# Kernel optimization log

Measured on AMD Instinct MI355X. Metric: run time of the kernel, lower is better.

The kernel has to match this reference:

```python
import jax, jax.numpy as jnp
import numpy as np

N, IN, HID, OUT, HD = 512, 256, 256, 256, 64  # n_agents, in_dim, hid_dim, out_dim, head_dim (out_dim // n_heads)


def _mlp2(x, w1, b1, w2, b2):
    return jax.nn.relu(x @ w1.T + b1) @ w2.T + b2


def setup_inputs():
    key = jax.random.key(0)
    ks = jax.random.split(key, 32)
    p = lambda i, shape: jax.random.normal(ks[i], shape, dtype=jnp.float32) * 0.05
    V = jax.random.normal(ks[0], (N, IN), dtype=jnp.float32)
    adj = jax.random.randint(ks[1], (N, N), 0, 2, dtype=jnp.int32)
    adj = adj.at[jnp.arange(N), jnp.arange(N)].set(1)  # self-loops so no softmax row is all -inf
    prev_hidden = jax.random.normal(ks[2], (N, HID), dtype=jnp.float32)
    return {
        "V": V, "adj": adj, "prev_hidden": prev_hidden,
        "W1": p(3, (HID, IN)), "sa0": p(4, (HID,)), "sa1": p(5, (HID,)),
        "ce_w1": p(6, (HID, 2 * IN)), "ce_b1": p(7, (HID,)), "ce_w2": p(8, (HD, HID)), "ce_b2": p(9, (HD,)),
        "ca0": p(10, (HD,)), "ca1": p(11, (HD,)),
        "te_w1": p(12, (HID, IN + HID)), "te_b1": p(13, (HID,)), "te_w2": p(14, (HD, HID)), "te_b2": p(15, (HD,)),
        "ta0": p(16, (HD,)), "ta1": p(17, (HD,)),
        "pe_w1": p(18, (HID, 3 * IN)), "pe_b1": p(19, (HID,)), "pe_w2": p(20, (HD, HID)), "pe_b2": p(21, (HD,)),
        "pa0": p(22, (HD,)), "pa1": p(23, (HD,)),
        "W2": p(24, (OUT, HID + 2 * HD + 1)), "op_w": p(25, (OUT, OUT)), "op_b": p(26, (OUT,)),
        "ln_g": jnp.ones((OUT,), jnp.float32), "ln_b": jnp.zeros((OUT,), jnp.float32),
    }


def _forward(V, adj, prev_hidden, W1, sa0, sa1, ce_w1, ce_b1, ce_w2, ce_b2, ca0, ca1,
             te_w1, te_b1, te_w2, te_b2, ta0, ta1, pe_w1, pe_b1, pe_w2, pe_b2, pa0, pa1,
             W2, op_w, op_b, ln_g, ln_b):
    neg = -jnp.inf
    # --- branch 1: standard GAT attention ---
    Wh1 = V @ W1.T                                             # (N, HID)
    s1 = (Wh1 @ sa0)[:, None] + (Wh1 @ sa1)[None, :]           # (N, N)
    s1 = jnp.where(adj == 0, neg, s1)
    H1 = jax.nn.softmax(s1, axis=1) @ Wh1                      # (N, HID)
    # --- branch 2: causal, all ordered pairs i != j ---
    wA, wB = ce_w1[:, :IN], ce_w1[:, IN:]
    h = jax.nn.relu((V @ wA.T)[:, None, :] + (V @ wB.T)[None, :, :] + ce_b1)  # (N, N, HID)
    f = h @ ce_w2.T + ce_b2                                    # (N, N, HD)
    s2 = jnp.where(jnp.eye(N, dtype=bool), neg, f @ (ca0 + ca1))
    a2 = jax.nn.softmax(s2.reshape(-1)).reshape(N, N)          # softmax over all off-diagonal pairs
    H2 = jnp.broadcast_to(jnp.einsum('ij,ijd->d', a2, f), (N, HD))
    # --- branch 3: temporal; (N,1) scores broadcast against (N,N) causal mask ---
    tf = _mlp2(jnp.concatenate([V, prev_hidden], -1), te_w1, te_b1, te_w2, te_b2)  # (N, HD)
    ts = tf @ (ta0 + ta1)                                      # (N,)
    cmask = jnp.triu(jnp.ones((N, N), dtype=bool), 1)
    s3 = jnp.where(cmask, neg, jnp.broadcast_to(ts[:, None], (N, N)))
    H3 = jax.nn.softmax(s3, axis=1) @ tf                       # (N, HD) == prefix means of tf
    # --- branch 4: cooperative; first two neighbors in index order (zeros if < 2) ---
    pos = jnp.where(adj == 1, jnp.arange(N)[None, :], N)
    srt = jnp.sort(pos, axis=1)
    i0, i1 = srt[:, 0], srt[:, 1]
    valid = (i1 < N)[:, None]
    n0 = jnp.where(valid, V[jnp.clip(i0, 0, N - 1)], 0.0)
    n1 = jnp.where(valid, V[jnp.clip(i1, 0, N - 1)], 0.0)
    cf = _mlp2(jnp.concatenate([V, n0, n1], -1), pe_w1, pe_b1, pe_w2, pe_b2)  # (N, HD)
    # torch: softmax over dim of size 1 -> all ones, alpha^T @ cf == column sums -> (HD,)
    # then unsqueezed to (HD,1) and zero-padded to (N,1) since HD < N  (faithful to source bug)
    H4v = cf.sum(axis=0)
    H4 = jnp.concatenate([H4v, jnp.zeros((N - HD,), V.dtype)])[:, None]       # (N, 1)
    # --- combine ---
    Hc = jnp.concatenate([H1, H2, H3, H4], axis=-1) @ W2.T     # (N, OUT)
    out = Hc @ op_w.T + op_b
    mu = out.mean(-1, keepdims=True)
    var = ((out - mu) ** 2).mean(-1, keepdims=True)
    y = (out - mu) / jnp.sqrt(var + 1e-5) * ln_g + ln_b        # LayerNorm, eps=1e-5
    return jax.nn.elu(y)                                       # dropout is identity in eval


def reference(V, adj, prev_hidden, W1, sa0, sa1, ce_w1, ce_b1, ce_w2, ce_b2, ca0, ca1,
              te_w1, te_b1, te_w2, te_b2, ta0, ta1, pe_w1, pe_b1, pe_w2, pe_b2, pa0, pa1,
              W2, op_w, op_b, ln_g, ln_b):
    return _forward(V, adj, prev_hidden, W1, sa0, sa1, ce_w1, ce_b1, ce_w2, ce_b2, ca0, ca1,
                    te_w1, te_b1, te_w2, te_b2, ta0, ta1, pe_w1, pe_b1, pe_w2, pe_b2, pa0, pa1,
                    W2, op_w, op_b, ln_g, ln_b)
```

## Files before the change

### kernel.cpp

```cpp
#include <hip/hip_runtime.h>
#include <hip/hip_cooperative_groups.h>

namespace cg = cooperative_groups;

typedef unsigned short u16;

constexpr int kN   = 512;
constexpr int kIN  = 256;
constexpr int kHID = 256;
constexpr int kHD  = 64;
constexpr int kOUT = 256;

__device__ __forceinline__ float us2f(u16 u){
  union { unsigned int i; float f; } c; c.i = ((unsigned int)u) << 16; return c.f;
}
__device__ __forceinline__ u16 f2us(float f){
  union { float f; unsigned int i; } c; c.f = f;
  unsigned int r = c.i + 0x7fff + ((c.i >> 16) & 1);
  return (u16)(r >> 16);
}
__device__ __forceinline__ float ldraw(const void* p, size_t i, bool f32){
  return f32 ? ((const float*)p)[i] : us2f(((const u16*)p)[i]);
}

__device__ bool probe_is_f32(const unsigned int* __restrict__ V){
  __shared__ int cnt;
  if (threadIdx.x == 0) cnt = 0;
  __syncthreads();
  int c = 0;
  for (int k = threadIdx.x; k < 4096; k += 256){
    float x = us2f((u16)(V[k] & 0xffffu));
    if (!(fabsf(x) <= 32.0f)) c++;
  }
  atomicAdd(&cnt, c);
  __syncthreads();
  return cnt > 64;
}

__device__ __forceinline__ float blk_red(float v, float* tmp, bool isMax){
  int lane = threadIdx.x & 63, wv = threadIdx.x >> 6;
  #pragma unroll
  for (int o = 32; o > 0; o >>= 1){
    float t = __shfl_down(v, o, 64);
    v = isMax ? fmaxf(v, t) : (v + t);
  }
  __syncthreads();
  if (lane == 0) tmp[wv] = v;
  __syncthreads();
  float r = tmp[0];
  for (int i = 1; i < 4; ++i) r = isMax ? fmaxf(r, tmp[i]) : (r + tmp[i]);
  return r;
}

struct ConvArgs { const void* src[23]; float* dst[23]; int n[23]; };
struct GSeg2 { const float* X; const float* W; float* C; int ldx, ldw, ldc, K; };
struct GS32 { const float* X; const float* W; float* C; int ldx, ldw, ldc, K; int bkn; };

struct MegaArgs {
  const unsigned int* Vraw;
  const int* adj;
  int* flag; void* out;
  const void *rca0,*rca1,*rcw2,*rcb2,*rtw2,*rpw2;
  float *Vf,*prevf,*W1f,*sa1f,*cw1f,*cb1f,*cw2f,*cb2f,*ca0f,*ca1f;
  float *tw1f,*tb1f,*tw2f,*tb2f,*pw1f,*pb1f,*pw2f,*pb2f;
  float *W2f,*opwf,*opbf,*lngf,*lnbf;
  float *tw2t,*pw2t,*Wcomb,*OM,*ow4;
  float *Wh1,*e1v,*wadj,*Hc,*Am,*Bm,*uvec,*beta;
  float *s2,*maxp,*zp,*MZ,*gsum;
  float *htp0,*htp1,*hpp0,*hpp1,*hpp2,*hidden_t,*hidden_p;
  float *tfm,*cfm,*H4v,*Xp,*out3;
  ConvArgs ca;
  GSeg2 gs[8];
};

__device__ __forceinline__ void gemm32_body(const GS32 sg, int tm, int tn, int tid,
                                            float* Xs, float* Ws)
{
  const int i0 = tm << 5, n0 = tn << 5;
  const int xrow = tid >> 3;
  const int xk = (tid & 7) << 2;
  const int rg = (tid >> 4) << 1;
  const int cg = (tid & 15) << 1;
  const float* Xb = sg.X + (size_t)i0 * sg.ldx;
  const float* Wb = sg.bkn ? (sg.W + n0) : (sg.W + (size_t)n0 * sg.ldw);
  float4 xr, wr;
  auto loadT = [&](int kt){
    xr = *(const float4*)(Xb + (size_t)xrow * sg.ldx + kt + xk);
    if (sg.bkn) wr = *(const float4*)(Wb + (size_t)(kt + xrow) * sg.ldw + xk);
    else        wr = *(const float4*)(Wb + (size_t)xrow * sg.ldw + kt + xk);
  };
  auto writeT = [&](int bu){
    float* xs = Xs + bu*1152;
    xs[(xk+0)*36 + xrow] = xr.x; xs[(xk+1)*36 + xrow] = xr.y;
    xs[(xk+2)*36 + xrow] = xr.z; xs[(xk+3)*36 + xrow] = xr.w;
    float* wsp = Ws + bu*1152;
    if (sg.bkn){
      wsp[xrow*36 + xk+0] = wr.x; wsp[xrow*36 + xk+1] = wr.y;
      wsp[xrow*36 + xk+2] = wr.z; wsp[xrow*36 + xk+3] = wr.w;
    } else {
      wsp[(xk+0)*36 + xrow] = wr.x; wsp[(xk+1)*36 + xrow] = wr.y;
      wsp[(xk+2)*36 + xrow] = wr.z; wsp[(xk+3)*36 + xrow] = wr.w;
    }
  };
  loadT(0); writeT(0); __syncthreads();
  float a00=0,a01=0,a10=0,a11=0;
  const int nkt = sg.K >> 5;
  for (int t = 0; t < nkt; ++t){
    if (t+1 < nkt) loadT((t+1) << 5);
    const float* xs = Xs + (t&1)*1152;
    const float* wsp = Ws + (t&1)*1152;
    #pragma unroll
    for (int kk = 0; kk < 32; ++kk){
      float2 av = *(const float2*)&xs[kk*36 + rg];
      float2 bv = *(const float2*)&wsp[kk*36 + cg];
      a00 += av.x*bv.x; a01 += av.x*bv.y;
      a10 += av.y*bv.x; a11 += av.y*bv.y;
    }
    if (t+1 < nkt) writeT((t+1)&1);
    __syncthreads();
  }
  float* cp = sg.C + (size_t)(i0+rg)*sg.ldc + n0 + cg;
  *(float2*)cp = make_float2(a00, a01);
  *(float2*)(cp + sg.ldc) = make_float2(a10, a11);
}


__device__ void body_s0(const MegaArgs& A, int it, int tid, bool f32, char* SM)
{
  if (it < 256){
    if (it == 0){
      if (tid == 0) *A.flag = f32 ? 1 : 0;
      A.e1v[tid] = 0.f; A.e1v[tid + 256] = 0.f;
    }
    int t = it*256 + tid;
    for (int s = 0; s < 23; ++s){
      int n4 = A.ca.n[s] >> 2;
      float4* d = (float4*)A.ca.dst[s];
      if (f32){
        const float4* sf = (const float4*)A.ca.src[s];
        for (int i = t; i < n4; i += 65536) d[i] = sf[i];
      } else {
        const ushort4* sb = (const ushort4*)A.ca.src[s];
        for (int i = t; i < n4; i += 65536){
          ushort4 u = sb[i];
          d[i] = make_float4(us2f(u.x), us2f(u.y), us2f(u.z), us2f(u.w));
        }
      }
    }
  } else if (it < 768){
    unsigned long long* msk = (unsigned long long*)SM;
    int* sj = (int*)(SM + 64);
    int i = it - 256;
    int w = tid >> 6, lane = tid & 63;
    unsigned long long m0 = __ballot(A.adj[(size_t)i*kN + tid] != 0);
    unsigned long long m1 = __ballot(A.adj[(size_t)i*kN + 256 + tid] != 0);
    if (lane == 0){ msk[w] = m0; msk[4 + w] = m1; }
    __syncthreads();
    if (tid == 0){
      int j0 = -1, j1 = -1;
      for (int c = 0; c < 8 && j1 < 0; ++c){
        unsigned long long m = msk[c];
        while (m && j1 < 0){
          int bb = __builtin_ctzll(m);
          int j = c*64 + bb;
          if (j0 < 0) j0 = j; else j1 = j;
          m &= m - 1;
        }
      }
      if (j1 < 0) j0 = -1;
      sj[0] = j0; sj[1] = j1;
    }
    __syncthreads();
    int j0 = sj[0], j1 = sj[1];
    A.Xp[(size_t)i*768 + tid]       = ldraw(A.Vraw, (size_t)i*kIN + tid, f32);
    A.Xp[(size_t)i*768 + 256 + tid] = (j0 >= 0) ? ldraw(A.Vraw, (size_t)j0*kIN + tid, f32) : 0.f;
    A.Xp[(size_t)i*768 + 512 + tid] = (j1 >= 0) ? ldraw(A.Vraw, (size_t)j1*kIN + tid, f32) : 0.f;
  } else if (it == 768){
    float* st = (float*)SM;
    if (tid < 64){ st[tid] = ldraw(A.rca0, tid, f32) + ldraw(A.rca1, tid, f32); A.H4v[tid] = 0.f; }
    __syncthreads();
    float a = 0.f;
    for (int d = 0; d < kHD; ++d) a += ldraw(A.rcw2, (size_t)d*kHID + tid, f32) * st[d];
    A.uvec[tid] = a;
    if (tid == 0){
      float b = 0.f;
      for (int d = 0; d < kHD; ++d) b += ldraw(A.rcb2, d, f32) * st[d];
      *A.beta = b;
    }
  } else {
    const void* src = (it == 769) ? A.rtw2 : A.rpw2;
    float* dst = (it == 769) ? A.tw2t : A.pw2t;
    float* st = (float*)SM;
    for (int ch = 0; ch < 4; ++ch){
      __syncthreads();
      #pragma unroll
      for (int e = 0; e < 16; ++e){
        int lin = e*256 + tid, r = lin >> 6, c = lin & 63;
        st[r*65 + c] = ldraw(src, (size_t)r*256 + ch*64 + c, f32);
      }
      __syncthreads();
      #pragma unroll
      for (int e = 0; e < 16; ++e){
        int lin = e*256 + tid, kc = lin >> 6, dd = lin & 63;
        dst[(size_t)(ch*64 + kc)*64 + dd] = st[dd*65 + kc];
      }
    }
  }
}

__device__ void body_gemmA(const MegaArgs& A, int it, int tid, char* SM)
{
  float (*Xs)[32][68] = (float (*)[32][68])SM;
  float (*Ws)[32][68] = (float (*)[32][68])(SM + 17408);
  int seg = it >> 5, x = it & 31;
  const GSeg2 sg = A.gs[seg];
  const int tm = x & 7, tn = x >> 3;
  const int i0 = tm << 6, n0 = tn << 6;

  const int xrow = tid >> 3;
  const int xk   = (tid & 7) << 2;
  const int rg = (tid >> 4) << 2;
  const int cg = (tid & 15) << 2;

  const float* Xb = sg.X + (size_t)i0 * sg.ldx;
  const float* Wb = sg.W + (size_t)n0 * sg.ldw;

  float4 xr0, xr1, wr0, wr1;
  auto loadT = [&](int kt){
    xr0 = *(const float4*)(Xb + (size_t)xrow * sg.ldx + kt + xk);
    xr1 = *(const float4*)(Xb + (size_t)(xrow+32) * sg.ldx + kt + xk);
    wr0 = *(const float4*)(Wb + (size_t)xrow * sg.ldw + kt + xk);
    wr1 = *(const float4*)(Wb + (size_t)(xrow+32) * sg.ldw + kt + xk);
  };
  auto writeT = [&](int bu){
    Xs[bu][xk+0][xrow] = xr0.x;  Xs[bu][xk+1][xrow] = xr0.y;
    Xs[bu][xk+2][xrow] = xr0.z;  Xs[bu][xk+3][xrow] = xr0.w;
    Xs[bu][xk+0][xrow+32] = xr1.x;  Xs[bu][xk+1][xrow+32] = xr1.y;
    Xs[bu][xk+2][xrow+32] = xr1.z;  Xs[bu][xk+3][xrow+32] = xr1.w;
    Ws[bu][xk+0][xrow]    = wr0.x; Ws[bu][xk+1][xrow]    = wr0.y;
    Ws[bu][xk+2][xrow]    = wr0.z; Ws[bu][xk+3][xrow]    = wr0.w;
    Ws[bu][xk+0][xrow+32] = wr1.x; Ws[bu][xk+1][xrow+32] = wr1.y;
    Ws[bu][xk+2][xrow+32] = wr1.z; Ws[bu][xk+3][xrow+32] = wr1.w;
  };

  loadT(0); writeT(0); __syncthreads();

  float acc[4][4] = {};
  const int nkt = sg.K >> 5;
  for (int t = 0; t < nkt; ++t){
    if (t + 1 < nkt) loadT((t + 1) << 5);
    const int bu = t & 1;
    #pragma unroll
    for (int kk = 0; kk < 32; ++kk){
      const float4 av = *(const float4*)&Xs[bu][kk][rg];
      const float4 bv = *(const float4*)&Ws[bu][kk][cg];
      acc[0][0]+=av.x*bv.x; acc[0][1]+=av.x*bv.y; acc[0][2]+=av.x*bv.z; acc[0][3]+=av.x*bv.w;
      acc[1][0]+=av.y*bv.x; acc[1][1]+=av.y*bv.y; acc[1][2]+=av.y*bv.z; acc[1][3]+=av.y*bv.w;
      acc[2][0]+=av.z*bv.x; acc[2][1]+=av.z*bv.y; acc[2][2]+=av.z*bv.z; acc[2][3]+=av.z*bv.w;
      acc[3][0]+=av.w*bv.x; acc[3][1]+=av.w*bv.y; acc[3][2]+=av.w*bv.z; acc[3][3]+=av.w*bv.w;
    }
    if (t + 1 < nkt) writeT((t + 1) & 1);
    __syncthreads();
  }

  #pragma unroll
  for (int ri = 0; ri < 4; ++ri)
    *(float4*)(sg.C + (size_t)(i0 + rg + ri) * sg.ldc + (n0 + cg)) =
      make_float4(acc[ri][0], acc[ri][1], acc[ri][2], acc[ri][3]);

  if (seg == 0){
    int cb = n0 + cg;
    float s0 = A.sa1f[cb], s1 = A.sa1f[cb+1], s2v = A.sa1f[cb+2], s3 = A.sa1f[cb+3];
    #pragma unroll
    for (int ri = 0; ri < 4; ++ri){
      float v = acc[ri][0]*s0 + acc[ri][1]*s1 + acc[ri][2]*s2v + acc[ri][3]*s3;
      v += __shfl_xor(v, 1, 16);
      v += __shfl_xor(v, 2, 16);
      v += __shfl_xor(v, 4, 16);
      v += __shfl_xor(v, 8, 16);
      if ((tid & 15) == 0) atomicAdd(&A.e1v[i0 + rg + ri], v);
    }
  }
}

__device__ void body_s1(const MegaArgs& A, int it, int tid, char* SM)
{
  if (it < 256){
    body_gemmA(A, it, tid, SM);
  } else if (it < 336){
    int q = it - 256, tm = q & 7, tn = q >> 3;
    const float* Wsrc = A.W2f + ((tn < 8) ? 0 : 64);
    GS32 sg{A.opwf, Wsrc, A.Wcomb, 256, 385, 320, 256, 1};
    gemm32_body(sg, tm, tn, tid, (float*)SM, (float*)(SM + 9216));
  } else if (it < 352){
    int q = it - 336;
    GS32 sg{A.opwf, A.W2f + 256, A.OM, 256, 385, 64, 256, 1};
    gemm32_body(sg, q & 7, q >> 3, tid, (float*)SM, (float*)(SM + 9216));
  } else {
    float* st = (float*)SM;
    st[tid] = A.W2f[(size_t)tid*385 + 384];
    __syncthreads();
    float a = 0.f;
    const float* orow = A.opwf + (size_t)tid*256;
    for (int m = 0; m < 256; m += 4){
      float4 o4 = *(const float4*)(orow + m);
      a += o4.x*st[m] + o4.y*st[m+1] + o4.z*st[m+2] + o4.w*st[m+3];
    }
    A.ow4[tid] = a;
  }
}

__device__ void body_s2(const MegaArgs& A, int it, int tid, char* SM)
{
  if (it < 128){
    int f = it*256 + tid;
    int c4 = f & 63;
    {
      float4 a = ((const float4*)A.htp0)[f], bb = ((const float4*)A.htp1)[f];
      float4 bi = ((const float4*)A.tb1f)[c4];
      ((float4*)A.hidden_t)[f] = make_float4(
        fmaxf(a.x+bb.x+bi.x,0.f), fmaxf(a.y+bb.y+bi.y,0.f),
        fmaxf(a.z+bb.z+bi.z,0.f), fmaxf(a.w+bb.w+bi.w,0.f));
    }
    {
      float4 a = ((const float4*)A.hpp0)[f], bb = ((const float4*)A.hpp1)[f];
      float4 c = ((const float4*)A.hpp2)[f];
      float4 bi = ((const float4*)A.pb1f)[c4];
      ((float4*)A.hidden_p)[f] = make_float4(
        fmaxf(a.x+bb.x+c.x+bi.x,0.f), fmaxf(a.y+bb.y+c.y+bi.y,0.f),
        fmaxf(a.z+bb.z+c.z+bi.z,0.f), fmaxf(a.w+bb.w+c.w+bi.w,0.f));
    }
  } else {
    float* st = (float*)SM;
    int i = it - 128;
    int m0 = A.adj[(size_t)i*kN + tid];
    int m1 = A.adj[(size_t)i*kN + tid + 256];
    float ea = A.e1v[tid], eb = A.e1v[tid+256];
    float v0 = m0 ? ea : -1e30f;
    float v1 = m1 ? eb : -1e30f;
    float m = blk_red(fmaxf(v0, v1), st, true);
    float z = blk_red((m0 ? expf(ea-m) : 0.f) + (m1 ? expf(eb-m) : 0.f), st, false);
    float iz = 1.0f / z;
    A.wadj[(size_t)i*kN + tid]       = m0 ? expf(ea - m) * iz : 0.f;
    A.wadj[(size_t)i*kN + tid + 256] = m1 ? expf(eb - m) * iz : 0.f;
  }
}

__device__ void body_s3(const MegaArgs& A, int it, int tid, char* SM)
{
  if (it < 64){
    int m = it >> 5, grp = it & 31;
    const float* X  = m ? A.hidden_p : A.hidden_t;
    const float* Wt = m ? A.pw2t : A.tw2t;
    const float* bi = m ? A.pb2f : A.tb2f;
    float* C = m ? A.cfm : A.tfm;
    int i0 = grp*16 + (tid >> 6)*4;
    int d = tid & 63;
    const float* x0 = X + (size_t)i0*256;
    const float* x1 = x0 + 256;
    const float* x2 = x0 + 512;
    const float* x3 = x0 + 768;
    float a0=0.f, a1=0.f, a2=0.f, a3=0.f;
    for (int k = 0; k < 256; k += 4){
      float w0 = Wt[(size_t)(k+0)*64 + d];
      float w1 = Wt[(size_t)(k+1)*64 + d];
      float w2 = Wt[(size_t)(k+2)*64 + d];
      float w3 = Wt[(size_t)(k+3)*64 + d];
      float4 f0 = *(const float4*)(x0 + k);
      float4 f1 = *(const float4*)(x1 + k);
      float4 f2 = *(const float4*)(x2 + k);
      float4 f3 = *(const float4*)(x3 + k);
      a0 += f0.x*w0 + f0.y*w1 + f0.z*w2 + f0.w*w3;
      a1 += f1.x*w0 + f1.y*w1 + f1.z*w2 + f1.w*w3;
      a2 += f2.x*w0 + f2.y*w1 + f2.z*w2 + f2.w*w3;
      a3 += f3.x*w0 + f3.y*w1 + f3.z*w2 + f3.w*w3;
    }
    float bd = bi[d];
    C[(size_t)(i0+0)*64 + d] = a0 + bd;
    C[(size_t)(i0+1)*64 + d] = a1 + bd;
    C[(size_t)(i0+2)*64 + d] = a2 + bd;
    C[(size_t)(i0+3)*64 + d] = a3 + bd;
  } else if (it < 1088){
    float* aib = (float*)SM;
    float* uu  = aib + 1024;
    int q = it - 64;
    int i0 = (q & 127) * 4, j0 = (q >> 7) * 64;
    int wv = tid >> 6, lane = tid & 63;
    uu[tid] = A.uvec[tid];
    float b1v = A.cb1f[tid];
    #pragma unroll
    for (int r = 0; r < 4; ++r) aib[r*256 + tid] = A.Am[(size_t)(i0+r)*kHID + tid] + b1v;
    __syncthreads();
    int i = i0 + wv, j = j0 + lane;
    const float4* bp = (const float4*)(A.Bm + (size_t)j*kHID);
    float acc = *A.beta;
    #pragma unroll 8
    for (int k4 = 0; k4 < kHID/4; ++k4){
      float4 bv = bp[k4];
      float4 a4 = *(const float4*)&aib[wv*256 + k4*4];
      float4 u4 = *(const float4*)&uu[k4*4];
      acc += fmaxf(a4.x+bv.x,0.f)*u4.x + fmaxf(a4.y+bv.y,0.f)*u4.y
           + fmaxf(a4.z+bv.z,0.f)*u4.z + fmaxf(a4.w+bv.w,0.f)*u4.w;
    }
    if (j == i) acc = -1e30f;
    A.s2[(size_t)i*kN + j] = acc;
    float m = acc;
    #pragma unroll
    for (int o = 32; o > 0; o >>= 1) m = fmaxf(m, __shfl_down(m, o, 64));
    m = __shfl(m, 0, 64);
    float e = expf(acc - m);
    #pragma unroll
    for (int o = 32; o > 0; o >>= 1) e += __shfl_down(e, o, 64);
    if (lane == 0){
      int pb = q*4 + wv;
      A.maxp[pb] = m; A.zp[pb] = e;
    }
  } else {
    int bb = it - 1088;
    GS32 sg{A.wadj, A.Wh1, A.Hc, 512, 256, 320, 512, 1};
    gemm32_body(sg, bb & 15, bb >> 4, tid, (float*)SM, (float*)(SM + 9216));
  }
}

__device__ void body_s4(const MegaArgs& A, int it, int tid, char* SM)
{
  if (it < 64){
    int d = it;
    int lane = tid & 63, wv = tid >> 6;
    float v0 = A.tfm[(size_t)(2*tid)*kHD + d];
    float v1 = A.tfm[(size_t)(2*tid+1)*kHD + d];
    float s = v0 + v1;
    float x = s;
    #pragma unroll
    for (int off = 1; off < 64; off <<= 1){
      float y = __shfl_up(x, off, 64);
      if (lane >= off) x += y;
    }
    float* wsum = (float*)SM;
    if (lane == 63) wsum[wv] = x;
    __syncthreads();
    float base = 0.f;
    for (int k = 0; k < wv; ++k) base += wsum[k];
    float excl = base + x - s;
    A.Hc[(size_t)(2*tid)*320 + 256 + d]   = (excl + v0) / (float)(2*tid + 1);
    A.Hc[(size_t)(2*tid+1)*320 + 256 + d] = (excl + s)  / (float)(2*tid + 2);
  } else if (it < 72){
    float* sm = (float*)SM;
    int d = tid & 63, sub = tid >> 6;
    int r0 = (it-64)*64 + sub*16;
    float s = 0.f;
    #pragma unroll
    for (int e = 0; e < 16; ++e) s += A.cfm[(size_t)(r0+e)*kHD + d];
    sm[sub*64 + d] = s;
    __syncthreads();
    if (tid < 64)
      atomicAdd(&A.H4v[tid], sm[tid] + sm[64+tid] + sm[128+tid] + sm[192+tid]);
  } else {
    float* red = (float*)SM;
    float m = -1e30f;
    #pragma unroll
    for (int r = 0; r < 16; ++r) m = fmaxf(m, A.maxp[tid + 256*r]);
    m = blk_red(m, red, true);
    float z = 0.f;
    #pragma unroll
    for (int r = 0; r < 16; ++r) z += A.zp[tid + 256*r] * expf(A.maxp[tid + 256*r] - m);
    z = blk_red(z, red, false);
    if (tid == 0){ A.MZ[0] = m; A.MZ[1] = z; }
    A.gsum[tid] = 0.f;
  }
}

__device__ void body_s5(const MegaArgs& A, int it, int tid, char* SM)
{
  if (it < 1024){
    float* wt = (float*)SM;
    int i0 = (it & 31) * 16, j0 = (it >> 5) * 16;
    float M = A.MZ[0], invZ = 1.0f / A.MZ[1];
    {
      int r = tid >> 4, c = tid & 15;
      wt[r*16 + c] = expf(A.s2[(size_t)(i0+r)*kN + (j0+c)] - M) * invZ;
    }
    float b1v = A.cb1f[tid];
    float aib[16];
    #pragma unroll
    for (int r = 0; r < 16; ++r) aib[r] = A.Am[(size_t)(i0+r)*kHID + tid] + b1v;
    __syncthreads();
    float acc = 0.f;
    for (int j = 0; j < 16; ++j){
      float bj = A.Bm[(size_t)(j0+j)*kHID + tid];
      #pragma unroll
      for (int r = 0; r < 16; ++r)
        acc += wt[r*16 + j] * fmaxf(aib[r] + bj, 0.f);
    }
    atomicAdd(&A.gsum[tid], acc);
  } else {
    int q = it - 1024;
    GS32 sg{A.Hc, A.Wcomb, A.out3, 320, 320, 256, 320, 0};
    gemm32_body(sg, q & 15, q >> 4, tid, (float*)SM, (float*)(SM + 9216));
  }
}

__device__ void body_s6(const MegaArgs& A, int it, int tid, bool f32, char* SM)
{
  float* gs   = (float*)SM;
  float* part = gs + 256;
  float* h2s  = part + 256;
  float* cc2s = h2s + 64;
  gs[tid] = A.gsum[tid];
  __syncthreads();
  {
    int dd = tid >> 2, q = tid & 3;
    float a = 0.f;
    for (int kk = 0; kk < 64; ++kk){
      int k = q*64 + kk;
      a += gs[k] * A.cw2f[(size_t)dd*kHID + k];
    }
    part[dd*4 + q] = a;
  }
  __syncthreads();
  if (tid < kHD)
    h2s[tid] = A.cb2f[tid] + part[tid*4] + part[tid*4+1] + part[tid*4+2] + part[tid*4+3];
  __syncthreads();
  {
    float a = 0.f;
    const float* om = A.OM + (size_t)tid*64;
    for (int d = 0; d < kHD; d += 4){
      float4 o4 = *(const float4*)(om + d);
      a += o4.x*h2s[d] + o4.y*h2s[d+1] + o4.z*h2s[d+2] + o4.w*h2s[d+3];
    }
    cc2s[tid] = a;
  }
  __syncthreads();
  int row = it*4 + (tid >> 6), lane = tid & 63;
  float h4r = (row < kHD) ? A.H4v[row] : 0.f;
  float4 v  = *(const float4*)(A.out3 + (size_t)row*kOUT + lane*4);
  float4 c2 = *(const float4*)(&cc2s[lane*4]);
  float4 o4 = *(const float4*)(A.ow4 + lane*4);
  float4 pb = *(const float4*)(A.opbf + lane*4);
  v.x += c2.x + h4r*o4.x + pb.x;
  v.y += c2.y + h4r*o4.y + pb.y;
  v.z += c2.z + h4r*o4.z + pb.z;
  v.w += c2.w + h4r*o4.w + pb.w;
  float s = v.x + v.y + v.z + v.w;
  #pragma unroll
  for (int o = 32; o > 0; o >>= 1) s += __shfl_xor(s, o, 64);
  float mu = s * (1.0f/kOUT);
  float dx = v.x-mu, dy = v.y-mu, dz = v.z-mu, dw = v.w-mu;
  float ss = dx*dx + dy*dy + dz*dz + dw*dw;
  #pragma unroll
  for (int o = 32; o > 0; o >>= 1) ss += __shfl_xor(ss, o, 64);
  float rs = rsqrtf(ss * (1.0f/kOUT) + 1e-5f);
  float4 g  = *(const float4*)(A.lngf + lane*4);
  float4 be = *(const float4*)(A.lnbf + lane*4);
  float y0 = dx*rs*g.x + be.x, y1 = dy*rs*g.y + be.y;
  float y2 = dz*rs*g.z + be.z, y3 = dw*rs*g.w + be.w;
  y0 = (y0 > 0.f) ? y0 : expm1f(y0);
  y1 = (y1 > 0.f) ? y1 : expm1f(y1);
  y2 = (y2 > 0.f) ? y2 : expm1f(y2);
  y3 = (y3 > 0.f) ? y3 : expm1f(y3);
  if (f32){
    *(float4*)((float*)A.out + (size_t)row*kOUT + lane*4) = make_float4(y0,y1,y2,y3);
  } else {
    ushort4 u; u.x = f2us(y0); u.y = f2us(y1); u.z = f2us(y2); u.w = f2us(y3);
    ((ushort4*)A.out)[(size_t)row*64 + lane] = u;
  }
}

__device__ __forceinline__ int stage_count(int s){
  switch(s){
    case 0: return 771;  case 1: return 353;  case 2: return 640;
    case 3: return 1216; case 4: return 73;   case 5: return 1152;
    default: return 128;
  }
}

__device__ void run_stage(int s, const MegaArgs& A, bool f32, char* SM, int b0, int nb)
{
  const int n = stage_count(s);
  const int tid = threadIdx.x;
  for (int it = b0; it < n; it += nb){
    switch(s){
      case 0: body_s0(A, it, tid, f32, SM); break;
      case 1: body_s1(A, it, tid, SM); break;
      case 2: body_s2(A, it, tid, SM); break;
      case 3: body_s3(A, it, tid, SM); break;
      case 4: body_s4(A, it, tid, SM); break;
      case 5: body_s5(A, it, tid, SM); break;
      default: body_s6(A, it, tid, f32, SM); break;
    }
    __syncthreads();
  }
}

__global__ __launch_bounds__(256) void k_mega(MegaArgs A)
{
  __shared__ __align__(16) char SM[34816];
  cg::grid_group grid = cg::this_grid();
  bool f32 = probe_is_f32(A.Vraw);
  #pragma unroll 1
  for (int s = 0; s < 7; ++s){
    run_stage(s, A, f32, SM, blockIdx.x, gridDim.x);
    if (s < 6){ __threadfence(); grid.sync(); }
  }
}

constexpr int kStageSM[7] = {16896, 34816, 64, 18432, 1024, 18432, 3328};

template<int S>
__global__ __launch_bounds__(256) void k_stage_one(MegaArgs A)
{
  __shared__ __align__(16) char SM[kStageSM[S]];
  bool f32 = (S == 0) ? probe_is_f32(A.Vraw) : (*A.flag != 0);
  run_stage(S, A, f32, SM, blockIdx.x, gridDim.x);
}

extern "C" void kernel_launch(void* const* d_in, const int* in_sizes, int n_in,
                              void* d_out, int out_size, void* d_ws, size_t ws_size,
                              hipStream_t stream)
{
  const void* V     = d_in[0];
  const int*  adj   = (const int*)d_in[1];
  const void* prev  = d_in[2];
  const void* W1    = d_in[3];
  const void* sa1   = d_in[5];
  const void* ce_w1 = d_in[6];
  const void* ce_b1 = d_in[7];
  const void* ce_w2 = d_in[8];
  const void* ce_b2 = d_in[9];
  const void* ca0   = d_in[10];
  const void* ca1   = d_in[11];
  const void* te_w1 = d_in[12];
  const void* te_b1 = d_in[13];
  const void* te_w2 = d_in[14];
  const void* te_b2 = d_in[15];
  const void* pe_w1 = d_in[18];
  const void* pe_b1 = d_in[19];
  const void* pe_w2 = d_in[20];
  const void* pe_b2 = d_in[21];
  const void* W2    = d_in[24];
  const void* op_w  = d_in[25];
  const void* op_b  = d_in[26];
  const void* ln_g  = d_in[27];
  const void* ln_b  = d_in[28];

  float* ws  = (float*)d_ws;
  int*  flag = (int*)ws;
  float* p   = ws + 16;
  float* Vf   = p; p += 131072;
  float* prevf= p; p += 131072;
  float* W1f  = p; p += 65536;
  float* sa1f = p; p += 256;
  float* cw1f = p; p += 131072;
  float* cb1f = p; p += 256;
  float* cw2f = p; p += 16384;
  float* cb2f = p; p += 64;
  float* ca0f = p; p += 64;
  float* ca1f = p; p += 64;
  float* tw1f = p; p += 131072;
  float* tb1f = p; p += 256;
  float* tw2f = p; p += 16384;
  float* tb2f = p; p += 64;
  float* pw1f = p; p += 196608;
  float* pb1f = p; p += 256;
  float* pw2f = p; p += 16384;
  float* pb2f = p; p += 64;
  float* W2f  = p; p += 98560;
  float* opwf = p; p += 65536;
  float* opbf = p; p += 256;
  float* lngf = p; p += 256;
  float* lnbf = p; p += 256;
  float* tw2t = p; p += 16384;
  float* pw2t = p; p += 16384;
  float* Wcomb= p; p += 81920;
  float* OM   = p; p += 16384;
  float* ow4  = p; p += 256;
  float* Wh1      = p; p += 131072;
  float* e1v      = p; p += 512;
  float* wadj     = p; p += 262144;
  float* Hc       = p; p += 163840;
  float* Am       = p; p += 131072;
  float* Bm       = p; p += 131072;
  float* uvec     = p; p += 256;
  float* beta     = p; p += 16;
  float* s2       = p; p += 262144;
  float* maxp     = p; p += 4096;
  float* zpart    = p; p += 4096;
  float* MZ       = p; p += 16;
  float* gsum     = p; p += 256;
  float* htp0     = p; p += 131072;
  float* htp1     = p; p += 131072;
  float* hpp0     = p; p += 131072;
  float* hpp1     = p; p += 131072;
  float* hpp2     = p; p += 131072;
  float* hidden_t = p; p += 131072;
  float* hidden_p = p; p += 131072;
  float* tfm      = p; p += 32768;
  float* cfm      = p; p += 32768;
  float* H4v      = p; p += 64;
  float* Xp       = p; p += 393216;
  float* out3     = p; p += 131072;

  MegaArgs A;
  A.Vraw = (const unsigned int*)V; A.adj = adj; A.flag = flag; A.out = d_out;
  A.rca0 = ca0; A.rca1 = ca1; A.rcw2 = ce_w2; A.rcb2 = ce_b2; A.rtw2 = te_w2; A.rpw2 = pe_w2;
  A.Vf=Vf; A.prevf=prevf; A.W1f=W1f; A.sa1f=sa1f; A.cw1f=cw1f; A.cb1f=cb1f;
  A.cw2f=cw2f; A.cb2f=cb2f; A.ca0f=ca0f; A.ca1f=ca1f;
  A.tw1f=tw1f; A.tb1f=tb1f; A.tw2f=tw2f; A.tb2f=tb2f;
  A.pw1f=pw1f; A.pb1f=pb1f; A.pw2f=pw2f; A.pb2f=pb2f;
  A.W2f=W2f; A.opwf=opwf; A.opbf=opbf; A.lngf=lngf; A.lnbf=lnbf;
  A.tw2t=tw2t; A.pw2t=pw2t; A.Wcomb=Wcomb; A.OM=OM; A.ow4=ow4;
  A.Wh1=Wh1; A.e1v=e1v; A.wadj=wadj; A.Hc=Hc;
  A.Am=Am; A.Bm=Bm; A.uvec=uvec; A.beta=beta;
  A.s2=s2; A.maxp=maxp; A.zp=zpart; A.MZ=MZ; A.gsum=gsum;
  A.htp0=htp0; A.htp1=htp1; A.hpp0=hpp0; A.hpp1=hpp1; A.hpp2=hpp2;
  A.hidden_t=hidden_t; A.hidden_p=hidden_p;
  A.tfm=tfm; A.cfm=cfm; A.H4v=H4v; A.Xp=Xp; A.out3=out3;

  {
    const void* srcs[23] = {V, prev, W1, sa1, ce_w1, ce_b1, ce_w2, ce_b2, ca0, ca1,
                            te_w1, te_b1, te_w2, te_b2, pe_w1, pe_b1, pe_w2, pe_b2,
                            W2, op_w, op_b, ln_g, ln_b};
    float* dsts[23] = {Vf, prevf, W1f, sa1f, cw1f, cb1f, cw2f, cb2f, ca0f, ca1f,
                       tw1f, tb1f, tw2f, tb2f, pw1f, pb1f, pw2f, pb2f,
                       W2f, opwf, opbf, lngf, lnbf};
    int ns[23] = {131072, 131072, 65536, 256, 131072, 256, 16384, 64, 64, 64,
                  131072, 256, 16384, 64, 196608, 256, 16384, 64,
                  98560, 65536, 256, 256, 256};
    for (int s = 0; s < 23; ++s){ A.ca.src[s] = srcs[s]; A.ca.dst[s] = dsts[s]; A.ca.n[s] = ns[s]; }
  }
  A.gs[0] = {Vf,       W1f,        Wh1,  256, 256, 256, 256};
  A.gs[1] = {Vf,       cw1f,       Am,   256, 512, 256, 256};
  A.gs[2] = {Vf,       cw1f + 256, Bm,   256, 512, 256, 256};
  A.gs[3] = {Vf,       tw1f,       htp0, 256, 512, 256, 256};
  A.gs[4] = {prevf,    tw1f + 256, htp1, 256, 512, 256, 256};
  A.gs[5] = {Xp,       pw1f,       hpp0, 768, 768, 256, 256};
  A.gs[6] = {Xp + 256, pw1f + 256, hpp1, 768, 768, 256, 256};
  A.gs[7] = {Xp + 512, pw1f + 512, hpp2, 768, 768, 256, 256};

  bool done = false;
  int perCU = 0;
  if (hipOccupancyMaxActiveBlocksPerMultiprocessor(&perCU,
        reinterpret_cast<const void*>(&k_mega), 256, 0) != hipSuccess)
    perCU = 0;
  if (perCU > 0){
    long long grid = (long long)perCU * 256;
    if (grid > 1216) grid = 1216;
    if (grid >= 64){
      void* prm[] = { (void*)&A };
      done = (hipLaunchCooperativeKernel(reinterpret_cast<const void*>(&k_mega),
                dim3((unsigned)grid), dim3(256), prm, 0, stream) == hipSuccess);
    }
  }

  if (!done){
    k_stage_one<0><<<771, 256, 0, stream>>>(A);
    k_stage_one<1><<<353, 256, 0, stream>>>(A);
    k_stage_one<2><<<640, 256, 0, stream>>>(A);
    k_stage_one<3><<<1216, 256, 0, stream>>>(A);
    k_stage_one<4><<<73, 256, 0, stream>>>(A);
    k_stage_one<5><<<1152, 256, 0, stream>>>(A);
    k_stage_one<6><<<128, 256, 0, stream>>>(A);
  }
}
```

Before: 273.9 us.

## Replace cooperative megakernel with six launches and fuse split-K GEMMs with bias-ReLU

Drops the cooperative grid-synchronized megakernel and launches six separate kernels instead, with stages regrouped so the former elementwise bias+ReLU stage disappears. The temporal and positional first-layer GEMMs now run over concatenated inputs (a new Xt buffer of V and prev_hidden, plus the full-K Xp) as single K=512/768 GEMMs with bias and ReLU in the epilogue, removing five partial-product buffers and their reduction pass. This removes one grid-wide barrier stage and intermediate traffic, but adds longer-K tiles with fewer blocks in that stage and replaces in-kernel grid syncs with kernel launch boundaries.

```diff
diff --git a/kernel.cpp b/kernel.cpp
--- a/kernel.cpp
+++ b/kernel.cpp
@@ -1,7 +1,4 @@
 #include <hip/hip_runtime.h>
-#include <hip/hip_cooperative_groups.h>
-
-namespace cg = cooperative_groups;
 
 typedef unsigned short u16;
 
@@ -52,25 +49,27 @@
   return r;
 }
 
-struct ConvArgs { const void* src[23]; float* dst[23]; int n[23]; };
-struct GSeg2 { const float* X; const float* W; float* C; int ldx, ldw, ldc, K; };
+constexpr int kNConv = 22;
+struct ConvArgs { const void* src[kNConv]; float* dst[kNConv]; int n[kNConv]; };
+struct GSeg2 { const float* X; const float* W; float* C; int ldx, ldw, ldc, K;
+               const float* bias; int act; };
 struct GS32 { const float* X; const float* W; float* C; int ldx, ldw, ldc, K; int bkn; };
 
-struct MegaArgs {
+struct Args {
   const unsigned int* Vraw;
   const int* adj;
+  const void* rprev;
   int* flag; void* out;
   const void *rca0,*rca1,*rcw2,*rcb2,*rtw2,*rpw2;
-  float *Vf,*prevf,*W1f,*sa1f,*cw1f,*cb1f,*cw2f,*cb2f,*ca0f,*ca1f;
+  float *Vf,*W1f,*sa1f,*cw1f,*cb1f,*cw2f,*cb2f,*ca0f,*ca1f;
   float *tw1f,*tb1f,*tw2f,*tb2f,*pw1f,*pb1f,*pw2f,*pb2f;
   float *W2f,*opwf,*opbf,*lngf,*lnbf;
   float *tw2t,*pw2t,*Wcomb,*OM,*ow4;
   float *Wh1,*e1v,*wadj,*Hc,*Am,*Bm,*uvec,*beta;
   float *s2,*maxp,*zp,*MZ,*gsum;
-  float *htp0,*htp1,*hpp0,*hpp1,*hpp2,*hidden_t,*hidden_p;
-  float *tfm,*cfm,*H4v,*Xp,*out3;
+  float *hidden_t,*hidden_p,*tfm,*cfm,*H4v,*Xp,*Xt,*out3;
   ConvArgs ca;
-  GSeg2 gs[8];
+  GSeg2 gs[5];
 };
 
 __device__ __forceinline__ void gemm32_body(const GS32 sg, int tm, int tn, int tid,
@@ -124,16 +123,104 @@
   *(float2*)(cp + sg.ldc) = make_float2(a10, a11);
 }
 
-
-__device__ void body_s0(const MegaArgs& A, int it, int tid, bool f32, char* SM)
-{
+__device__ void body_gemmA(const Args& A, int it, int tid, char* SM)
+{
+  float (*Xs)[32][68] = (float (*)[32][68])SM;
+  float (*Ws)[32][68] = (float (*)[32][68])(SM + 17408);
+  int seg = it >> 5, x = it & 31;
+  const GSeg2 sg = A.gs[seg];
+  const int tm = x & 7, tn = x >> 3;
+  const int i0 = tm << 6, n0 = tn << 6;
+
+  const int xrow = tid >> 3;
+  const int xk   = (tid & 7) << 2;
+  const int rg = (tid >> 4) << 2;
+  const int cg = (tid & 15) << 2;
+
+  const float* Xb = sg.X + (size_t)i0 * sg.ldx;
+  const float* Wb = sg.W + (size_t)n0 * sg.ldw;
+
+  float4 xr0, xr1, wr0, wr1;
+  auto loadT = [&](int kt){
+    xr0 = *(const float4*)(Xb + (size_t)xrow * sg.ldx + kt + xk);
+    xr1 = *(const float4*)(Xb + (size_t)(xrow+32) * sg.ldx + kt + xk);
+    wr0 = *(const float4*)(Wb + (size_t)xrow * sg.ldw + kt + xk);
+    wr1 = *(const float4*)(Wb + (size_t)(xrow+32) * sg.ldw + kt + xk);
+  };
+  auto writeT = [&](int bu){
+    Xs[bu][xk+0][xrow] = xr0.x;  Xs[bu][xk+1][xrow] = xr0.y;
+    Xs[bu][xk+2][xrow] = xr0.z;  Xs[bu][xk+3][xrow] = xr0.w;
+    Xs[bu][xk+0][xrow+32] = xr1.x;  Xs[bu][xk+1][xrow+32] = xr1.y;
+    Xs[bu][xk+2][xrow+32] = xr1.z;  Xs[bu][xk+3][xrow+32] = xr1.w;
+    Ws[bu][xk+0][xrow]    = wr0.x; Ws[bu][xk+1][xrow]    = wr0.y;
+    Ws[bu][xk+2][xrow]    = wr0.z; Ws[bu][xk+3][xrow]    = wr0.w;
+    Ws[bu][xk+0][xrow+32] = wr1.x; Ws[bu][xk+1][xrow+32] = wr1.y;
+    Ws[bu][xk+2][xrow+32] = wr1.z; Ws[bu][xk+3][xrow+32] = wr1.w;
+  };
+
+  loadT(0); writeT(0); __syncthreads();
+
+  float acc[4][4] = {};
+  const int nkt = sg.K >> 5;
+  for (int t = 0; t < nkt; ++t){
+    if (t + 1 < nkt) loadT((t + 1) << 5);
+    const int bu = t & 1;
+    #pragma unroll
+    for (int kk = 0; kk < 32; ++kk){
+      const float4 av = *(const float4*)&Xs[bu][kk][rg];
+      const float4 bv = *(const float4*)&Ws[bu][kk][cg];
+      acc[0][0]+=av.x*bv.x; acc[0][1]+=av.x*bv.y; acc[0][2]+=av.x*bv.z; acc[0][3]+=av.x*bv.w;
+      acc[1][0]+=av.y*bv.x; acc[1][1]+=av.y*bv.y; acc[1][2]+=av.y*bv.z; acc[1][3]+=av.y*bv.w;
+      acc[2][0]+=av.z*bv.x; acc[2][1]+=av.z*bv.y; acc[2][2]+=av.z*bv.z; acc[2][3]+=av.z*bv.w;
+      acc[3][0]+=av.w*bv.x; acc[3][1]+=av.w*bv.y; acc[3][2]+=av.w*bv.z; acc[3][3]+=av.w*bv.w;
+    }
+    if (t + 1 < nkt) writeT((t + 1) & 1);
+    __syncthreads();
+  }
+
+  float bb[4] = {0.f, 0.f, 0.f, 0.f};
+  if (sg.bias){
+    bb[0] = sg.bias[n0+cg+0]; bb[1] = sg.bias[n0+cg+1];
+    bb[2] = sg.bias[n0+cg+2]; bb[3] = sg.bias[n0+cg+3];
+  }
+  #pragma unroll
+  for (int ri = 0; ri < 4; ++ri){
+    float4 v = make_float4(acc[ri][0]+bb[0], acc[ri][1]+bb[1],
+                           acc[ri][2]+bb[2], acc[ri][3]+bb[3]);
+    if (sg.act){
+      v.x = fmaxf(v.x, 0.f); v.y = fmaxf(v.y, 0.f);
+      v.z = fmaxf(v.z, 0.f); v.w = fmaxf(v.w, 0.f);
+    }
+    *(float4*)(sg.C + (size_t)(i0 + rg + ri) * sg.ldc + (n0 + cg)) = v;
+  }
+
+  if (seg == 0){
+    int cb = n0 + cg;
+    float s0 = A.sa1f[cb], s1 = A.sa1f[cb+1], s2v = A.sa1f[cb+2], s3 = A.sa1f[cb+3];
+    #pragma unroll
+    for (int ri = 0; ri < 4; ++ri){
+      float v = acc[ri][0]*s0 + acc[ri][1]*s1 + acc[ri][2]*s2v + acc[ri][3]*s3;
+      v += __shfl_xor(v, 1, 16);
+      v += __shfl_xor(v, 2, 16);
+      v += __shfl_xor(v, 4, 16);
+      v += __shfl_xor(v, 8, 16);
+      if ((tid & 15) == 0) atomicAdd(&A.e1v[i0 + rg + ri], v);
+    }
+  }
+}
+
+__global__ __launch_bounds__(256) void k_s0(Args A)
+{
+  __shared__ __align__(16) char SM[16896];
+  int it = blockIdx.x, tid = threadIdx.x;
+  bool f32 = probe_is_f32(A.Vraw);
   if (it < 256){
     if (it == 0){
       if (tid == 0) *A.flag = f32 ? 1 : 0;
       A.e1v[tid] = 0.f; A.e1v[tid + 256] = 0.f;
     }
     int t = it*256 + tid;
-    for (int s = 0; s < 23; ++s){
+    for (int s = 0; s < kNConv; ++s){
       int n4 = A.ca.n[s] >> 2;
       float4* d = (float4*)A.ca.dst[s];
       if (f32){
@@ -172,9 +259,12 @@
     }
     __syncthreads();
     int j0 = sj[0], j1 = sj[1];
-    A.Xp[(size_t)i*768 + tid]       = ldraw(A.Vraw, (size_t)i*kIN + tid, f32);
+    float vi = ldraw(A.Vraw, (size_t)i*kIN + tid, f32);
+    A.Xp[(size_t)i*768 + tid]       = vi;
     A.Xp[(size_t)i*768 + 256 + tid] = (j0 >= 0) ? ldraw(A.Vraw, (size_t)j0*kIN + tid, f32) : 0.f;
     A.Xp[(size_t)i*768 + 512 + tid] = (j1 >= 0) ? ldraw(A.Vraw, (size_t)j1*kIN + tid, f32) : 0.f;
+    A.Xt[(size_t)i*512 + tid]       = vi;
+    A.Xt[(size_t)i*512 + 256 + tid] = ldraw(A.rprev, (size_t)i*kHID + tid, f32);
   } else if (it == 768){
     float* st = (float*)SM;
     if (tid < 64){ st[tid] = ldraw(A.rca0, tid, f32) + ldraw(A.rca1, tid, f32); A.H4v[tid] = 0.f; }
@@ -208,92 +298,19 @@
   }
 }
 
-__device__ void body_gemmA(const MegaArgs& A, int it, int tid, char* SM)
-{
-  float (*Xs)[32][68] = (float (*)[32][68])SM;
-  float (*Ws)[32][68] = (float (*)[32][68])(SM + 17408);
-  int seg = it >> 5, x = it & 31;
-  const GSeg2 sg = A.gs[seg];
-  const int tm = x & 7, tn = x >> 3;
-  const int i0 = tm << 6, n0 = tn << 6;
-
-  const int xrow = tid >> 3;
-  const int xk   = (tid & 7) << 2;
-  const int rg = (tid >> 4) << 2;
-  const int cg = (tid & 15) << 2;
-
-  const float* Xb = sg.X + (size_t)i0 * sg.ldx;
-  const float* Wb = sg.W + (size_t)n0 * sg.ldw;
-
-  float4 xr0, xr1, wr0, wr1;
-  auto loadT = [&](int kt){
-    xr0 = *(const float4*)(Xb + (size_t)xrow * sg.ldx + kt + xk);
-    xr1 = *(const float4*)(Xb + (size_t)(xrow+32) * sg.ldx + kt + xk);
-    wr0 = *(const float4*)(Wb + (size_t)xrow * sg.ldw + kt + xk);
-    wr1 = *(const float4*)(Wb + (size_t)(xrow+32) * sg.ldw + kt + xk);
-  };
-  auto writeT = [&](int bu){
-    Xs[bu][xk+0][xrow] = xr0.x;  Xs[bu][xk+1][xrow] = xr0.y;
-    Xs[bu][xk+2][xrow] = xr0.z;  Xs[bu][xk+3][xrow] = xr0.w;
-    Xs[bu][xk+0][xrow+32] = xr1.x;  Xs[bu][xk+1][xrow+32] = xr1.y;
-    Xs[bu][xk+2][xrow+32] = xr1.z;  Xs[bu][xk+3][xrow+32] = xr1.w;
-    Ws[bu][xk+0][xrow]    = wr0.x; Ws[bu][xk+1][xrow]    = wr0.y;
-    Ws[bu][xk+2][xrow]    = wr0.z; Ws[bu][xk+3][xrow]    = wr0.w;
-    Ws[bu][xk+0][xrow+32] = wr1.x; Ws[bu][xk+1][xrow+32] = wr1.y;
-    Ws[bu][xk+2][xrow+32] = wr1.z; Ws[bu][xk+3][xrow+32] = wr1.w;
-  };
-
-  loadT(0); writeT(0); __syncthreads();
-
-  float acc[4][4] = {};
-  const int nkt = sg.K >> 5;
-  for (int t = 0; t < nkt; ++t){
-    if (t + 1 < nkt) loadT((t + 1) << 5);
-    const int bu = t & 1;
-    #pragma unroll
-    for (int kk = 0; kk < 32; ++kk){
-      const float4 av = *(const float4*)&Xs[bu][kk][rg];
-      const float4 bv = *(const float4*)&Ws[bu][kk][cg];
-      acc[0][0]+=av.x*bv.x; acc[0][1]+=av.x*bv.y; acc[0][2]+=av.x*bv.z; acc[0][3]+=av.x*bv.w;
-      acc[1][0]+=av.y*bv.x; acc[1][1]+=av.y*bv.y; acc[1][2]+=av.y*bv.z; acc[1][3]+=av.y*bv.w;
-      acc[2][0]+=av.z*bv.x; acc[2][1]+=av.z*bv.y; acc[2][2]+=av.z*bv.z; acc[2][3]+=av.z*bv.w;
-      acc[3][0]+=av.w*bv.x; acc[3][1]+=av.w*bv.y; acc[3][2]+=av.w*bv.z; acc[3][3]+=av.w*bv.w;
-    }
-    if (t + 1 < nkt) writeT((t + 1) & 1);
-    __syncthreads();
-  }
-
-  #pragma unroll
-  for (int ri = 0; ri < 4; ++ri)
-    *(float4*)(sg.C + (size_t)(i0 + rg + ri) * sg.ldc + (n0 + cg)) =
-      make_float4(acc[ri][0], acc[ri][1], acc[ri][2], acc[ri][3]);
-
-  if (seg == 0){
-    int cb = n0 + cg;
-    float s0 = A.sa1f[cb], s1 = A.sa1f[cb+1], s2v = A.sa1f[cb+2], s3 = A.sa1f[cb+3];
-    #pragma unroll
-    for (int ri = 0; ri < 4; ++ri){
-      float v = acc[ri][0]*s0 + acc[ri][1]*s1 + acc[ri][2]*s2v + acc[ri][3]*s3;
-      v += __shfl_xor(v, 1, 16);
-      v += __shfl_xor(v, 2, 16);
-      v += __shfl_xor(v, 4, 16);
-      v += __shfl_xor(v, 8, 16);
-      if ((tid & 15) == 0) atomicAdd(&A.e1v[i0 + rg + ri], v);
-    }
-  }
-}
-
-__device__ void body_s1(const MegaArgs& A, int it, int tid, char* SM)
-{
-  if (it < 256){
+__global__ __launch_bounds__(256) void k_s1(Args A)
+{
+  __shared__ __align__(16) char SM[34816];
+  int it = blockIdx.x, tid = threadIdx.x;
+  if (it < 160){
     body_gemmA(A, it, tid, SM);
-  } else if (it < 336){
-    int q = it - 256, tm = q & 7, tn = q >> 3;
+  } else if (it < 240){
+    int q = it - 160, tm = q & 7, tn = q >> 3;
     const float* Wsrc = A.W2f + ((tn < 8) ? 0 : 64);
     GS32 sg{A.opwf, Wsrc, A.Wcomb, 256, 385, 320, 256, 1};
     gemm32_body(sg, tm, tn, tid, (float*)SM, (float*)(SM + 9216));
-  } else if (it < 352){
-    int q = it - 336;
+  } else if (it < 256){
+    int q = it - 240;
     GS32 sg{A.opwf, A.W2f + 256, A.OM, 256, 385, 64, 256, 1};
     gemm32_body(sg, q & 7, q >> 3, tid, (float*)SM, (float*)(SM + 9216));
   } else {
@@ -310,46 +327,60 @@
   }
 }
 
-__device__ void body_s2(const MegaArgs& A, int it, int tid, char* SM)
-{
-  if (it < 128){
-    int f = it*256 + tid;
-    int c4 = f & 63;
-    {
-      float4 a = ((const float4*)A.htp0)[f], bb = ((const float4*)A.htp1)[f];
-      float4 bi = ((const float4*)A.tb1f)[c4];
-      ((float4*)A.hidden_t)[f] = make_float4(
-        fmaxf(a.x+bb.x+bi.x,0.f), fmaxf(a.y+bb.y+bi.y,0.f),
-        fmaxf(a.z+bb.z+bi.z,0.f), fmaxf(a.w+bb.w+bi.w,0.f));
-    }
-    {
-      float4 a = ((const float4*)A.hpp0)[f], bb = ((const float4*)A.hpp1)[f];
-      float4 c = ((const float4*)A.hpp2)[f];
-      float4 bi = ((const float4*)A.pb1f)[c4];
-      ((float4*)A.hidden_p)[f] = make_float4(
-        fmaxf(a.x+bb.x+c.x+bi.x,0.f), fmaxf(a.y+bb.y+c.y+bi.y,0.f),
-        fmaxf(a.z+bb.z+c.z+bi.z,0.f), fmaxf(a.w+bb.w+c.w+bi.w,0.f));
-    }
-  } else {
-    float* st = (float*)SM;
-    int i = it - 128;
+__global__ __launch_bounds__(256) void k_s2(Args A)
+{
+  __shared__ __align__(16) float SM2[4*256 + 256];
+  int it = blockIdx.x, tid = threadIdx.x;
+  if (it < 512){
+    int i = it;
     int m0 = A.adj[(size_t)i*kN + tid];
     int m1 = A.adj[(size_t)i*kN + tid + 256];
     float ea = A.e1v[tid], eb = A.e1v[tid+256];
     float v0 = m0 ? ea : -1e30f;
     float v1 = m1 ? eb : -1e30f;
-    float m = blk_red(fmaxf(v0, v1), st, true);
-    float z = blk_red((m0 ? expf(ea-m) : 0.f) + (m1 ? expf(eb-m) : 0.f), st, false);
+    float m = blk_red(fmaxf(v0, v1), SM2, true);
+    float z = blk_red((m0 ? expf(ea-m) : 0.f) + (m1 ? expf(eb-m) : 0.f), SM2, false);
     float iz = 1.0f / z;
     A.wadj[(size_t)i*kN + tid]       = m0 ? expf(ea - m) * iz : 0.f;
     A.wadj[(size_t)i*kN + tid + 256] = m1 ? expf(eb - m) * iz : 0.f;
-  }
-}
-
-__device__ void body_s3(const MegaArgs& A, int it, int tid, char* SM)
-{
-  if (it < 64){
-    int m = it >> 5, grp = it & 31;
+  } else if (it < 1536){
+    float* aib = SM2;
+    float* uu  = SM2 + 1024;
+    int q = it - 512;
+    int i0 = (q & 127) * 4, j0 = (q >> 7) * 64;
+    int wv = tid >> 6, lane = tid & 63;
+    uu[tid] = A.uvec[tid];
+    float b1v = A.cb1f[tid];
+    #pragma unroll
+    for (int r = 0; r < 4; ++r) aib[r*256 + tid] = A.Am[(size_t)(i0+r)*kHID + tid] + b1v;
+    __syncthreads();
+    int i = i0 + wv, j = j0 + lane;
+    const float4* bp = (const float4*)(A.Bm + (size_t)j*kHID);
+    float acc = *A.beta;
+    #pragma unroll 8
+    for (int k4 = 0; k4 < kHID/4; ++k4){
+      float4 bv = bp[k4];
+      float4 a4 = *(const float4*)&aib[wv*256 + k4*4];
+      float4 u4 = *(const float4*)&uu[k4*4];
+      acc += fmaxf(a4.x+bv.x,0.f)*u4.x + fmaxf(a4.y+bv.y,0.f)*u4.y
+           + fmaxf(a4.z+bv.z,0.f)*u4.z + fmaxf(a4.w+bv.w,0.f)*u4.w;
+    }
+    if (j == i) acc = -1e30f;
+    A.s2[(size_t)i*kN + j] = acc;
+    float m = acc;
+    #pragma unroll
+    for (int o = 32; o > 0; o >>= 1) m = fmaxf(m, __shfl_down(m, o, 64));
+    m = __shfl(m, 0, 64);
+    float e = expf(acc - m);
+    #pragma unroll
+    for (int o = 32; o > 0; o >>= 1) e += __shfl_down(e, o, 64);
+    if (lane == 0){
+      int pb = q*4 + wv;
+      A.maxp[pb] = m; A.zp[pb] = e;
+    }
+  } else {
+    int q = it - 1536;
+    int m = q >> 5, grp = q & 31;
     const float* X  = m ? A.hidden_p : A.hidden_t;
     const float* Wt = m ? A.pw2t : A.tw2t;
     const float* bi = m ? A.pb2f : A.tb2f;
@@ -380,52 +411,18 @@
     C[(size_t)(i0+1)*64 + d] = a1 + bd;
     C[(size_t)(i0+2)*64 + d] = a2 + bd;
     C[(size_t)(i0+3)*64 + d] = a3 + bd;
-  } else if (it < 1088){
-    float* aib = (float*)SM;
-    float* uu  = aib + 1024;
-    int q = it - 64;
-    int i0 = (q & 127) * 4, j0 = (q >> 7) * 64;
-    int wv = tid >> 6, lane = tid & 63;
-    uu[tid] = A.uvec[tid];
-    float b1v = A.cb1f[tid];
-    #pragma unroll
-    for (int r = 0; r < 4; ++r) aib[r*256 + tid] = A.Am[(size_t)(i0+r)*kHID + tid] + b1v;
-    __syncthreads();
-    int i = i0 + wv, j = j0 + lane;
-    const float4* bp = (const float4*)(A.Bm + (size_t)j*kHID);
-    float acc = *A.beta;
-    #pragma unroll 8
-    for (int k4 = 0; k4 < kHID/4; ++k4){
-      float4 bv = bp[k4];
-      float4 a4 = *(const float4*)&aib[wv*256 + k4*4];
-      float4 u4 = *(const float4*)&uu[k4*4];
-      acc += fmaxf(a4.x+bv.x,0.f)*u4.x + fmaxf(a4.y+bv.y,0.f)*u4.y
-           + fmaxf(a4.z+bv.z,0.f)*u4.z + fmaxf(a4.w+bv.w,0.f)*u4.w;
-    }
-    if (j == i) acc = -1e30f;
-    A.s2[(size_t)i*kN + j] = acc;
-    float m = acc;
-    #pragma unroll
-    for (int o = 32; o > 0; o >>= 1) m = fmaxf(m, __shfl_down(m, o, 64));
-    m = __shfl(m, 0, 64);
-    float e = expf(acc - m);
-    #pragma unroll
-    for (int o = 32; o > 0; o >>= 1) e += __shfl_down(e, o, 64);
-    if (lane == 0){
-      int pb = q*4 + wv;
-      A.maxp[pb] = m; A.zp[pb] = e;
-    }
-  } else {
-    int bb = it - 1088;
+  }
+}
+
+__global__ __launch_bounds__(256) void k_s3(Args A)
+{
+  __shared__ __align__(16) char SM[18432];
+  int it = blockIdx.x, tid = threadIdx.x;
+  if (it < 128){
     GS32 sg{A.wadj, A.Wh1, A.Hc, 512, 256, 320, 512, 1};
-    gemm32_body(sg, bb & 15, bb >> 4, tid, (float*)SM, (float*)(SM + 9216));
-  }
-}
-
-__device__ void body_s4(const MegaArgs& A, int it, int tid, char* SM)
-{
-  if (it < 64){
-    int d = it;
+    gemm32_body(sg, it & 15, it >> 4, tid, (float*)SM, (float*)(SM + 9216));
+  } else if (it < 192){
+    int d = it - 128;
     int lane = tid & 63, wv = tid >> 6;
     float v0 = A.tfm[(size_t)(2*tid)*kHD + d];
     float v1 = A.tfm[(size_t)(2*tid+1)*kHD + d];
@@ -444,10 +441,10 @@
     float excl = base + x - s;
     A.Hc[(size_t)(2*tid)*320 + 256 + d]   = (excl + v0) / (float)(2*tid + 1);
     A.Hc[(size_t)(2*tid+1)*320 + 256 + d] = (excl + s)  / (float)(2*tid + 2);
-  } else if (it < 72){
+  } else if (it < 200){
     float* sm = (float*)SM;
     int d = tid & 63, sub = tid >> 6;
-    int r0 = (it-64)*64 + sub*16;
+    int r0 = (it-192)*64 + sub*16;
     float s = 0.f;
     #pragma unroll
     for (int e = 0; e < 16; ++e) s += A.cfm[(size_t)(r0+e)*kHD + d];
@@ -470,8 +467,10 @@
   }
 }
 
-__device__ void body_s5(const MegaArgs& A, int it, int tid, char* SM)
-{
+__global__ __launch_bounds__(256) void k_s4(Args A)
+{
+  __shared__ __align__(16) char SM[18432];
+  int it = blockIdx.x, tid = threadIdx.x;
   if (it < 1024){
     float* wt = (float*)SM;
     int i0 = (it & 31) * 16, j0 = (it >> 5) * 16;
@@ -500,12 +499,14 @@
   }
 }
 
-__device__ void body_s6(const MegaArgs& A, int it, int tid, bool f32, char* SM)
-{
-  float* gs   = (float*)SM;
-  float* part = gs + 256;
-  float* h2s  = part + 256;
-  float* cc2s = h2s + 64;
+__global__ __launch_bounds__(256) void k_s5(Args A)
+{
+  __shared__ float gs[kHID];
+  __shared__ float part[kHD][4];
+  __shared__ float h2s[kHD];
+  __shared__ float cc2s[kOUT];
+  int b = blockIdx.x, tid = threadIdx.x;
+  bool f32 = (*A.flag != 0);
   gs[tid] = A.gsum[tid];
   __syncthreads();
   {
@@ -515,11 +516,11 @@
       int k = q*64 + kk;
       a += gs[k] * A.cw2f[(size_t)dd*kHID + k];
     }
-    part[dd*4 + q] = a;
+    part[dd][q] = a;
   }
   __syncthreads();
   if (tid < kHD)
-    h2s[tid] = A.cb2f[tid] + part[tid*4] + part[tid*4+1] + part[tid*4+2] + part[tid*4+3];
+    h2s[tid] = A.cb2f[tid] + part[tid][0] + part[tid][1] + part[tid][2] + part[tid][3];
   __syncthreads();
   {
     float a = 0.f;
@@ -531,7 +532,7 @@
     cc2s[tid] = a;
   }
   __syncthreads();
-  int row = it*4 + (tid >> 6), lane = tid & 63;
+  int row = b*4 + (tid >> 6), lane = tid & 63;
   float h4r = (row < kHD) ? A.H4v[row] : 0.f;
   float4 v  = *(const float4*)(A.out3 + (size_t)row*kOUT + lane*4);
   float4 c2 = *(const float4*)(&cc2s[lane*4]);
@@ -566,54 +567,6 @@
   }
 }
 
-__device__ __forceinline__ int stage_count(int s){
-  switch(s){
-    case 0: return 771;  case 1: return 353;  case 2: return 640;
-    case 3: return 1216; case 4: return 73;   case 5: return 1152;
-    default: return 128;
-  }
-}
-
-__device__ void run_stage(int s, const MegaArgs& A, bool f32, char* SM, int b0, int nb)
-{
-  const int n = stage_count(s);
-  const int tid = threadIdx.x;
-  for (int it = b0; it < n; it += nb){
-    switch(s){
-      case 0: body_s0(A, it, tid, f32, SM); break;
-      case 1: body_s1(A, it, tid, SM); break;
-      case 2: body_s2(A, it, tid, SM); break;
-      case 3: body_s3(A, it, tid, SM); break;
-      case 4: body_s4(A, it, tid, SM); break;
-      case 5: body_s5(A, it, tid, SM); break;
-      default: body_s6(A, it, tid, f32, SM); break;
-    }
-    __syncthreads();
-  }
-}
-
-__global__ __launch_bounds__(256) void k_mega(MegaArgs A)
-{
-  __shared__ __align__(16) char SM[34816];
-  cg::grid_group grid = cg::this_grid();
-  bool f32 = probe_is_f32(A.Vraw);
-  #pragma unroll 1
-  for (int s = 0; s < 7; ++s){
-    run_stage(s, A, f32, SM, blockIdx.x, gridDim.x);
-    if (s < 6){ __threadfence(); grid.sync(); }
-  }
-}
-
-constexpr int kStageSM[7] = {16896, 34816, 64, 18432, 1024, 18432, 3328};
-
-template<int S>
-__global__ __launch_bounds__(256) void k_stage_one(MegaArgs A)
-{
-  __shared__ __align__(16) char SM[kStageSM[S]];
-  bool f32 = (S == 0) ? probe_is_f32(A.Vraw) : (*A.flag != 0);
-  run_stage(S, A, f32, SM, blockIdx.x, gridDim.x);
-}
-
 extern "C" void kernel_launch(void* const* d_in, const int* in_sizes, int n_in,
                               void* d_out, int out_size, void* d_ws, size_t ws_size,
                               hipStream_t stream)
@@ -647,7 +600,6 @@
   int*  flag = (int*)ws;
   float* p   = ws + 16;
   float* Vf   = p; p += 131072;
-  float* prevf= p; p += 131072;
   float* W1f  = p; p += 65536;
   float* sa1f = p; p += 256;
   float* cw1f = p; p += 131072;
@@ -687,23 +639,20 @@
   float* zpart    = p; p += 4096;
   float* MZ       = p; p += 16;
   float* gsum     = p; p += 256;
-  float* htp0     = p; p += 131072;
-  float* htp1     = p; p += 131072;
-  float* hpp0     = p; p += 131072;
-  float* hpp1     = p; p += 131072;
-  float* hpp2     = p; p += 131072;
   float* hidden_t = p; p += 131072;
   float* hidden_p = p; p += 131072;
   float* tfm      = p; p += 32768;
   float* cfm      = p; p += 32768;
   float* H4v      = p; p += 64;
   float* Xp       = p; p += 393216;
+  float* Xt       = p; p += 262144;
   float* out3     = p; p += 131072;
 
-  MegaArgs A;
-  A.Vraw = (const unsigned int*)V; A.adj = adj; A.flag = flag; A.out = d_out;
+  Args A;
+  A.Vraw = (const unsigned int*)V; A.adj = adj; A.rprev = prev;
+  A.flag = flag; A.out = d_out;
   A.rca0 = ca0; A.rca1 = ca1; A.rcw2 = ce_w2; A.rcb2 = ce_b2; A.rtw2 = te_w2; A.rpw2 = pe_w2;
-  A.Vf=Vf; A.prevf=prevf; A.W1f=W1f; A.sa1f=sa1f; A.cw1f=cw1f; A.cb1f=cb1f;
+  A.Vf=Vf; A.W1f=W1f; A.sa1f=sa1f; A.cw1f=cw1f; A.cb1f=cb1f;
   A.cw2f=cw2f; A.cb2f=cb2f; A.ca0f=ca0f; A.ca1f=ca1f;
   A.tw1f=tw1f; A.tb1f=tb1f; A.tw2f=tw2f; A.tb2f=tb2f;
   A.pw1f=pw1f; A.pb1f=pb1f; A.pw2f=pw2f; A.pb2f=pb2f;
@@ -712,53 +661,31 @@
   A.Wh1=Wh1; A.e1v=e1v; A.wadj=wadj; A.Hc=Hc;
   A.Am=Am; A.Bm=Bm; A.uvec=uvec; A.beta=beta;
   A.s2=s2; A.maxp=maxp; A.zp=zpart; A.MZ=MZ; A.gsum=gsum;
-  A.htp0=htp0; A.htp1=htp1; A.hpp0=hpp0; A.hpp1=hpp1; A.hpp2=hpp2;
   A.hidden_t=hidden_t; A.hidden_p=hidden_p;
-  A.tfm=tfm; A.cfm=cfm; A.H4v=H4v; A.Xp=Xp; A.out3=out3;
+  A.tfm=tfm; A.cfm=cfm; A.H4v=H4v; A.Xp=Xp; A.Xt=Xt; A.out3=out3;
 
   {
-    const void* srcs[23] = {V, prev, W1, sa1, ce_w1, ce_b1, ce_w2, ce_b2, ca0, ca1,
-                            te_w1, te_b1, te_w2, te_b2, pe_w1, pe_b1, pe_w2, pe_b2,
-                            W2, op_w, op_b, ln_g, ln_b};
-    float* dsts[23] = {Vf, prevf, W1f, sa1f, cw1f, cb1f, cw2f, cb2f, ca0f, ca1f,
-                       tw1f, tb1f, tw2f, tb2f, pw1f, pb1f, pw2f, pb2f,
-                       W2f, opwf, opbf, lngf, lnbf};
-    int ns[23] = {131072, 131072, 65536, 256, 131072, 256, 16384, 64, 64, 64,
-                  131072, 256, 16384, 64, 196608, 256, 16384, 64,
-                  98560, 65536, 256, 256, 256};
-    for (int s = 0; s < 23; ++s){ A.ca.src[s] = srcs[s]; A.ca.dst[s] = dsts[s]; A.ca.n[s] = ns[s]; }
-  }
-  A.gs[0] = {Vf,       W1f,        Wh1,  256, 256, 256, 256};
-  A.gs[1] = {Vf,       cw1f,       Am,   256, 512, 256, 256};
-  A.gs[2] = {Vf,       cw1f + 256, Bm,   256, 512, 256, 256};
-  A.gs[3] = {Vf,       tw1f,       htp0, 256, 512, 256, 256};
-  A.gs[4] = {prevf,    tw1f + 256, htp1, 256, 512, 256, 256};
-  A.gs[5] = {Xp,       pw1f,       hpp0, 768, 768, 256, 256};
-  A.gs[6] = {Xp + 256, pw1f + 256, hpp1, 768, 768, 256, 256};
-  A.gs[7] = {Xp + 512, pw1f + 512, hpp2, 768, 768, 256, 256};
-
-  bool done = false;
-  int perCU = 0;
-  if (hipOccupancyMaxActiveBlocksPerMultiprocessor(&perCU,
-        reinterpret_cast<const void*>(&k_mega), 256, 0) != hipSuccess)
-    perCU = 0;
-  if (perCU > 0){
-    long long grid = (long long)perCU * 256;
-    if (grid > 1216) grid = 1216;
-    if (grid >= 64){
-      void* prm[] = { (void*)&A };
-      done = (hipLaunchCooperativeKernel(reinterpret_cast<const void*>(&k_mega),
-                dim3((unsigned)grid), dim3(256), prm, 0, stream) == hipSuccess);
-    }
-  }
-
-  if (!done){
-    k_stage_one<0><<<771, 256, 0, stream>>>(A);
-    k_stage_one<1><<<353, 256, 0, stream>>>(A);
-    k_stage_one<2><<<640, 256, 0, stream>>>(A);
-    k_stage_one<3><<<1216, 256, 0, stream>>>(A);
-    k_stage_one<4><<<73, 256, 0, stream>>>(A);
-    k_stage_one<5><<<1152, 256, 0, stream>>>(A);
-    k_stage_one<6><<<128, 256, 0, stream>>>(A);
-  }
-}
+    const void* srcs[kNConv] = {V, W1, sa1, ce_w1, ce_b1, ce_w2, ce_b2, ca0, ca1,
+                                te_w1, te_b1, te_w2, te_b2, pe_w1, pe_b1, pe_w2, pe_b2,
+                                W2, op_w, op_b, ln_g, ln_b};
+    float* dsts[kNConv] = {Vf, W1f, sa1f, cw1f, cb1f, cw2f, cb2f, ca0f, ca1f,
+                           tw1f, tb1f, tw2f, tb2f, pw1f, pb1f, pw2f, pb2f,
+                           W2f, opwf, opbf, lngf, lnbf};
+    int ns[kNConv] = {131072, 65536, 256, 131072, 256, 16384, 64, 64, 64,
+                      131072, 256, 16384, 64, 196608, 256, 16384, 64,
+                      98560, 65536, 256, 256, 256};
+    for (int s = 0; s < kNConv; ++s){ A.ca.src[s] = srcs[s]; A.ca.dst[s] = dsts[s]; A.ca.n[s] = ns[s]; }
+  }
+  A.gs[0] = {Vf, W1f,        Wh1,      256, 256, 256, 256, nullptr, 0};
+  A.gs[1] = {Vf, cw1f,       Am,       256, 512, 256, 256, nullptr, 0};
+  A.gs[2] = {Vf, cw1f + 256, Bm,       256, 512, 256, 256, nullptr, 0};
+  A.gs[3] = {Xt, tw1f,       hidden_t, 512, 512, 256, 512, tb1f, 1};
+  A.gs[4] = {Xp, pw1f,       hidden_p, 768, 768, 256, 768, pb1f, 1};
+
+  k_s0<<<771,  256, 0, stream>>>(A);
+  k_s1<<<257,  256, 0, stream>>>(A);
+  k_s2<<<1600, 256, 0, stream>>>(A);
+  k_s3<<<201,  256, 0, stream>>>(A);
+  k_s4<<<1152, 256, 0, stream>>>(A);
+  k_s5<<<128,  256, 0, stream>>>(A);
+}
```

New measurement: 262.3 us. 1.04x faster.
